# Optimization experiments

Hardware: AMD Instinct MI355X
Metric: run time of the kernel (lower is better)

Reference implementation:

```python
import jax, jax.numpy as jnp
import numpy as np
import math

B, S, D, H, L, F = 32, 512, 512, 8, 4, 1024
TD = 4 * D  # time embedding dim
DH = D // H
SCALE = 1.0 / math.sqrt(DH)


def _ln(x, g, b):
    m = jnp.mean(x, -1, keepdims=True)
    v = jnp.var(x, -1, keepdims=True)
    return (x - m) * jax.lax.rsqrt(v + 1e-5) * g + b


def setup_inputs() -> dict:
    key = jax.random.key(0)
    ks = jax.random.split(key, 12)
    w = lambda k, shp: jax.random.normal(k, shp, dtype=jnp.float32) * 0.02
    return {
        "x": jax.random.normal(ks[0], (B, S, D), dtype=jnp.float32),
        "time": jax.random.uniform(ks[1], (B,), dtype=jnp.float32) * 1000.0,
        "time_w1": w(ks[2], (TD, D)), "time_b1": jnp.zeros((TD,), jnp.float32),
        "time_w2": w(ks[3], (TD, TD)), "time_b2": jnp.zeros((TD,), jnp.float32),
        "Wq": w(ks[4], (L, D, D)), "bq": jnp.zeros((L, D), jnp.float32),
        "Wk": w(ks[5], (L, D, D)), "bk": jnp.zeros((L, D), jnp.float32),
        "Wv": w(ks[6], (L, D, D)), "bv": jnp.zeros((L, D), jnp.float32),
        "Wo": w(ks[7], (L, D, D)), "bo": jnp.zeros((L, D), jnp.float32),
        "attn_g": jnp.ones((L, D), jnp.float32), "attn_b": jnp.zeros((L, D), jnp.float32),
        "ffn_g": jnp.ones((L, D), jnp.float32), "ffn_b": jnp.zeros((L, D), jnp.float32),
        "W1": w(ks[8], (L, 2 * F, D)), "b1": jnp.zeros((L, 2 * F), jnp.float32),
        "W2": w(ks[9], (L, D, F)), "b2": jnp.zeros((L, D), jnp.float32),
        "Wt": w(ks[10], (L, 4 * F, TD)), "bt": jnp.zeros((L, 4 * F), jnp.float32),
        "head_g": jnp.ones((D,), jnp.float32), "head_b": jnp.zeros((D,), jnp.float32),
        "Wh": w(ks[11], (D, D)), "bh": jnp.zeros((D,), jnp.float32),
    }


def _forward(x, time, time_w1, time_b1, time_w2, time_b2,
             Wq, bq, Wk, bk, Wv, bv, Wo, bo,
             attn_g, attn_b, ffn_g, ffn_b,
             W1, b1, W2, b2, Wt, bt,
             head_g, head_b, Wh, bh):
    Bsz = x.shape[0]
    # --- sinusoidal time embedding + time MLP ---
    half = D // 2
    freqs = jnp.exp(jnp.arange(half, dtype=jnp.float32) * (-math.log(10000.0) / (half - 1)))
    e = time[:, None] * freqs[None, :]
    temb = jnp.concatenate([jnp.sin(e), jnp.cos(e)], axis=-1)  # [B, D]
    temb = jax.nn.gelu(temb @ time_w1.T + time_b1, approximate=False) @ time_w2.T + time_b2  # [B, 4D]
    for i in range(L):
        # attention (prenorm; block 0 skips the norm since first_prenormalization=False)
        h = x if i == 0 else _ln(x, attn_g[i], attn_b[i])
        q = (h @ Wq[i].T + bq[i]).reshape(Bsz, S, H, DH)
        k = (h @ Wk[i].T + bk[i]).reshape(Bsz, S, H, DH)
        v = (h @ Wv[i].T + bv[i]).reshape(Bsz, S, H, DH)
        logits = jnp.einsum('bqhd,bkhd->bhqk', q, k) * SCALE
        probs = jax.nn.softmax(logits, axis=-1)
        o = jnp.einsum('bhqk,bkhd->bqhd', probs, v).reshape(Bsz, S, D)
        x = x + (o @ Wo[i].T + bo[i])
        # FFN with FiLM time conditioning and ReGLU activation
        h = _ln(x, ffn_g[i], ffn_b[i])
        h1 = h @ W1[i].T + b1[i]  # [B, S, 2F]
        tm = jax.nn.silu(temb) @ Wt[i].T + bt[i]  # [B, 4F]
        scale, shift = jnp.split(tm[:, None, :], 2, axis=-1)  # each [B, 1, 2F]
        h1 = h1 * (scale + 1.0) + shift
        a, g = jnp.split(h1, 2, axis=-1)  # ReGLU: a * relu(g)
        x = x + ((a * jax.nn.relu(g)) @ W2[i].T + b2[i])
    # head: last token -> LayerNorm -> ReLU -> Linear
    z = _ln(x[:, -1], head_g, head_b)
    return jax.nn.relu(z) @ Wh.T + bh


def reference(x, time, time_w1, time_b1, time_w2, time_b2,
              Wq, bq, Wk, bk, Wv, bv, Wo, bo,
              attn_g, attn_b, ffn_g, ffn_b,
              W1, b1, W2, b2, Wt, bt,
              head_g, head_b, Wh, bh):
    return _forward(x, time, time_w1, time_b1, time_w2, time_b2,
                    Wq, bq, Wk, bk, Wv, bv, Wo, bo,
                    attn_g, attn_b, ffn_g, ffn_b,
                    W1, b1, W2, b2, Wt, bt,
                    head_g, head_b, Wh, bh)
```

## Files before the change

### kernel.cpp

```cpp
#include <hip/hip_runtime.h>
#include <math.h>

typedef __bf16 bf16_t;
typedef __bf16 bf16x8 __attribute__((ext_vector_type(8)));
typedef float f32x4 __attribute__((ext_vector_type(4)));

__device__ __forceinline__ void gload_lds16(const void* g, void* l) {
    __builtin_amdgcn_global_load_lds(
        (const __attribute__((address_space(1))) void*)g,
        (__attribute__((address_space(3))) void*)l, 16, 0, 0);
}

__global__ void k_f2b(const float* __restrict__ in, bf16_t* __restrict__ out, int n8) {
    int idx = blockIdx.x * 256 + threadIdx.x;
    if (idx >= n8) return;
    const float* p = in + (size_t)idx * 8;
    bf16x8 r;
#pragma unroll
    for (int j = 0; j < 8; j++) r[j] = (bf16_t)p[j];
    *(bf16x8*)(out + (size_t)idx * 8) = r;
}

__global__ void k_f2b_s(const float* __restrict__ in, bf16_t* __restrict__ out,
                        int seg8, int dstride8) {
    int idx = blockIdx.x * 256 + threadIdx.x;
    int seg = idx / seg8, rem = idx - seg * seg8;
    const float* p = in + (size_t)idx * 8;
    bf16x8 r;
#pragma unroll
    for (int j = 0; j < 8; j++) r[j] = (bf16_t)p[j];
    *(bf16x8*)(out + ((size_t)seg * dstride8 + rem) * 8) = r;
}

__global__ void k_time_embed(const float* __restrict__ time, float* __restrict__ temb0) {
    int b = blockIdx.x;
    int j = threadIdx.x;
    float f = __expf((float)j * -0.036118981458730134f);
    float e = time[b] * f;
    temb0[(size_t)b * 512 + j] = sinf(e);
    temb0[(size_t)b * 512 + 256 + j] = cosf(e);
}

template<bool DO_NORM, bool IN32>
__global__ void k_ln(const void* __restrict__ xp, const float* __restrict__ g,
                     const float* __restrict__ b, bf16_t* __restrict__ out) {
    int row = blockIdx.x * 4 + (threadIdx.x >> 6);
    int lane = threadIdx.x & 63;
    float vals[8];
    if (IN32) {
        const float* xr = (const float*)xp + (size_t)row * 512 + lane * 8;
        float4 v0 = *(const float4*)xr;
        float4 v1 = *(const float4*)(xr + 4);
        vals[0] = v0.x; vals[1] = v0.y; vals[2] = v0.z; vals[3] = v0.w;
        vals[4] = v1.x; vals[5] = v1.y; vals[6] = v1.z; vals[7] = v1.w;
    } else {
        bf16x8 xv = *(const bf16x8*)((const bf16_t*)xp + (size_t)row * 512 + lane * 8);
#pragma unroll
        for (int j = 0; j < 8; j++) vals[j] = (float)xv[j];
    }
    bf16x8 r;
    if (DO_NORM) {
        float s = 0.f, sq = 0.f;
#pragma unroll
        for (int j = 0; j < 8; j++) { s += vals[j]; sq += vals[j] * vals[j]; }
#pragma unroll
        for (int m = 1; m < 64; m <<= 1) { s += __shfl_xor(s, m, 64); sq += __shfl_xor(sq, m, 64); }
        float mean = s * (1.0f / 512.0f);
        float var = sq * (1.0f / 512.0f) - mean * mean;
        float rstd = rsqrtf(var + 1e-5f);
        float4 g0 = *(const float4*)(g + lane * 8);
        float4 g1 = *(const float4*)(g + lane * 8 + 4);
        float4 b0 = *(const float4*)(b + lane * 8);
        float4 b1 = *(const float4*)(b + lane * 8 + 4);
        float gs[8] = {g0.x, g0.y, g0.z, g0.w, g1.x, g1.y, g1.z, g1.w};
        float bs[8] = {b0.x, b0.y, b0.z, b0.w, b1.x, b1.y, b1.z, b1.w};
#pragma unroll
        for (int j = 0; j < 8; j++) r[j] = (bf16_t)((vals[j] - mean) * rstd * gs[j] + bs[j]);
    } else {
#pragma unroll
        for (int j = 0; j < 8; j++) r[j] = (bf16_t)vals[j];
    }
    *(bf16x8*)(out + (size_t)row * 512 + lane * 8) = r;
}

__global__ void k_head_prep(const bf16_t* __restrict__ x, const float* __restrict__ g,
                            const float* __restrict__ b, float* __restrict__ z) {
    int row = blockIdx.x * 4 + (threadIdx.x >> 6);
    int lane = threadIdx.x & 63;
    bf16x8 xv = *(const bf16x8*)(x + ((size_t)row * 512 + 511) * 512 + lane * 8);
    float vals[8];
#pragma unroll
    for (int j = 0; j < 8; j++) vals[j] = (float)xv[j];
    float s = 0.f, sq = 0.f;
#pragma unroll
    for (int j = 0; j < 8; j++) { s += vals[j]; sq += vals[j] * vals[j]; }
#pragma unroll
    for (int m = 1; m < 64; m <<= 1) { s += __shfl_xor(s, m, 64); sq += __shfl_xor(sq, m, 64); }
    float mean = s * (1.0f / 512.0f);
    float var = sq * (1.0f / 512.0f) - mean * mean;
    float rstd = rsqrtf(var + 1e-5f);
    float o[8];
#pragma unroll
    for (int j = 0; j < 8; j++) {
        float gv = g[lane * 8 + j], bv = b[lane * 8 + j];
        o[j] = fmaxf((vals[j] - mean) * rstd * gv + bv, 0.0f);
    }
    float* zr = z + (size_t)row * 512 + lane * 8;
    *(float4*)zr = make_float4(o[0], o[1], o[2], o[3]);
    *(float4*)(zr + 4) = make_float4(o[4], o[5], o[6], o[7]);
}

template<int ACT, int K, bool OUTB>
__global__ __launch_bounds__(256, 2)
void k_gemm_tm(const float* __restrict__ A, const float* __restrict__ W,
               const float* __restrict__ bias, void* __restrict__ outp, int N) {
    __shared__ float Asm[32][516];
    const int t = threadIdx.x;
    const int kq = t & 7, rw = (t >> 3) & 7, bh = t >> 6;
    const int n0 = blockIdx.x * 32;
    float acc[4][8] = {};
    for (int k0 = 0; k0 < K; k0 += 512) {
        __syncthreads();
#pragma unroll
        for (int i = 0; i < 16; i++) {
            int fid = t + i * 256;
            int row = fid >> 7, cc = (fid & 127) << 2;
            *(float4*)&Asm[row][cc] = *(const float4*)&A[(size_t)row * K + k0 + cc];
        }
        __syncthreads();
#pragma unroll 4
        for (int j = 0; j < 16; j++) {
            int kk = kq * 4 + j * 32;
            float4 w4[4];
#pragma unroll
            for (int r = 0; r < 4; r++)
                w4[r] = *(const float4*)&W[(size_t)(n0 + rw + r * 8) * K + k0 + kk];
#pragma unroll
            for (int b = 0; b < 8; b++) {
                float4 a4 = *(const float4*)&Asm[bh * 8 + b][kk];
#pragma unroll
                for (int r = 0; r < 4; r++)
                    acc[r][b] += a4.x * w4[r].x + a4.y * w4[r].y + a4.z * w4[r].z + a4.w * w4[r].w;
            }
        }
    }
#pragma unroll
    for (int m = 1; m < 8; m <<= 1)
#pragma unroll
        for (int r = 0; r < 4; r++)
#pragma unroll
            for (int b = 0; b < 8; b++)
                acc[r][b] += __shfl_xor(acc[r][b], m, 64);
    if (kq == 0) {
#pragma unroll
        for (int r = 0; r < 4; r++) {
            int n = n0 + rw + r * 8;
            float bv = bias[n];
#pragma unroll
            for (int b = 0; b < 8; b++) {
                float v = acc[r][b] + bv;
                if (ACT == 1) v = 0.5f * v * (1.0f + erff(v * 0.70710678118654752f));
                if (ACT == 2) v = v / (1.0f + __expf(-v));
                if (OUTB) ((bf16_t*)outp)[(size_t)(bh * 8 + b) * N + n] = (bf16_t)v;
                else      ((float*)outp)[(size_t)(bh * 8 + b) * N + n] = v;
            }
        }
    }
}

__global__ void k_fill_tmt(const float* __restrict__ bt, float* __restrict__ tm_t) {
    int i = blockIdx.x * 256 + threadIdx.x;
    tm_t[i] = bt[i >> 5];
}

__global__ __launch_bounds__(256, 4)
void k_gemm_wt(const float* __restrict__ Wt, const bf16_t* __restrict__ t2s_b,
               float* __restrict__ tm_t) {
    __shared__ __align__(16) bf16_t Abuf[64 * 64];
    __shared__ __align__(16) bf16_t Bbuf[32 * 64];
    const int tid = threadIdx.x;
    const int m0 = blockIdx.x * 64;
    const int k0 = blockIdx.y * 512;
    const int lane = tid & 63, wave = tid >> 6;
    const int arow = tid >> 2, aseg = tid & 3;
    const int brow = tid >> 3, bseg = tid & 7;
    const int aswz = (arow & 7) << 4;
    const char* Bg = (const char*)t2s_b + (size_t)brow * 4096 + ((bseg * 16) ^ ((brow & 7) << 4));
    char* BbL = (char*)Bbuf + tid * 16;
    const float* Ar0 = Wt + (size_t)(m0 + arow) * 2048 + k0 + aseg * 16;
    f32x4 acc[2] = {};
    for (int kk0 = 0; kk0 < 512; kk0 += 64) {
        float4 a4[4];
#pragma unroll
        for (int i = 0; i < 4; i++) a4[i] = *(const float4*)(Ar0 + kk0 + i * 4);
        __syncthreads();
        gload_lds16(Bg + (size_t)(k0 + kk0) * 2, BbL);
        bf16x8 c0, c1;
#pragma unroll
        for (int i = 0; i < 4; i++) {
            const float* af = (const float*)&a4[i];
#pragma unroll
            for (int j = 0; j < 4; j++) {
                if (i < 2) c0[i * 4 + j] = (bf16_t)af[j];
                else       c1[(i - 2) * 4 + j] = (bf16_t)af[j];
            }
        }
        int base = arow * 128 + aseg * 32;
        *(bf16x8*)((char*)Abuf + (base ^ aswz)) = c0;
        *(bf16x8*)((char*)Abuf + ((base + 16) ^ aswz)) = c1;
        __syncthreads();
#pragma unroll
        for (int kk = 0; kk < 2; kk++) {
            int ar = wave * 16 + (lane & 15);
            bf16x8 af = *(const bf16x8*)((const char*)Abuf + ar * 128 +
                        ((kk * 64 + (lane >> 4) * 16) ^ ((ar & 7) << 4)));
#pragma unroll
            for (int j = 0; j < 2; j++) {
                int br = j * 16 + (lane & 15);
                bf16x8 bfr = *(const bf16x8*)((const char*)Bbuf + br * 128 +
                             ((kk * 64 + (lane >> 4) * 16) ^ ((br & 7) << 4)));
                acc[j] = __builtin_amdgcn_mfma_f32_16x16x32_bf16(af, bfr, acc[j], 0, 0, 0);
            }
        }
    }
#pragma unroll
    for (int j = 0; j < 2; j++)
#pragma unroll
        for (int r = 0; r < 4; r++) {
            int mrow = m0 + wave * 16 + (lane >> 4) * 4 + r;
            atomicAdd(&tm_t[(size_t)mrow * 32 + j * 16 + (lane & 15)], acc[j][r]);
        }
}

enum { EPI_QKV = 0, EPI_RESID = 1, EPI_FILMGLU = 2 };

template<int EPI, int K, int NBY, int BM, bool RS32>
__global__ __launch_bounds__(BM * 2, 4)
void k_gemm_bt(const bf16_t* __restrict__ A, const bf16_t* __restrict__ W,
               const float* __restrict__ bias, const float* __restrict__ bias2,
               const float* __restrict__ bias3,
               void* __restrict__ out0, const void* __restrict__ rsp, void* __restrict__ out2,
               const float* __restrict__ tm) {
    constexpr int T   = BM * 2;
    constexpr int RPR = BM / 4;
    constexpr int BR  = 512 / BM;
    __shared__ __align__(16) bf16_t Abuf[BM * 64];
    __shared__ __align__(16) bf16_t Bbuf[128 * 64];
    const int tid = threadIdx.x;
    const int cpx = gridDim.x >> 3;
    const int wg = (blockIdx.x & 7) * cpx + (blockIdx.x >> 3);
    const int bx = wg / NBY;
    const int by = wg - bx * NBY;
    const int m0 = bx * BM;
    const int lane = tid & 63;
    const int wid = tid >> 6;
    const int wrM = (wid >> 1) * 64;
    const int wN  = wid & 1;
    const int wc  = wN * 64;

    const int srow = tid >> 3;
    const int goff = ((tid & 7) * 16) ^ ((srow & 7) << 4);
    const char* Ag = (const char*)A;
    const char* Wg = (const char*)W;
    char* AbL = (char*)Abuf + tid * 16;
    char* BbL = (char*)Bbuf + tid * 16;
    int growB[BR];
#pragma unroll
    for (int i = 0; i < BR; i++) {
        int r = srow + i * RPR;
        if (EPI == EPI_FILMGLU) {
            int half = (r >> 5) & 1;
            int base = by * 64 + (r >> 6) * 32 + (r & 31);
            growB[i] = half * 1024 + base;
        } else {
            growB[i] = by * 128 + r;
        }
    }

    f32x4 acc[4][4] = {};
    for (int k0 = 0; k0 < K * 2; k0 += 128) {
        __syncthreads();
#pragma unroll
        for (int i = 0; i < 4; i++)
            gload_lds16(Ag + (size_t)(m0 + srow + i * RPR) * (K * 2) + k0 + goff, AbL + i * (T * 16));
#pragma unroll
        for (int i = 0; i < BR; i++)
            gload_lds16(Wg + (size_t)growB[i] * (K * 2) + k0 + goff, BbL + i * (T * 16));
        __syncthreads();
#pragma unroll
        for (int kk = 0; kk < 2; kk++) {
            bf16x8 af[4], bfr[4];
#pragma unroll
            for (int i = 0; i < 4; i++) {
                int ar = wrM + i * 16 + (lane & 15);
                af[i] = *(const bf16x8*)((const char*)Abuf + ar * 128 +
                         ((kk * 64 + (lane >> 4) * 16) ^ ((ar & 7) << 4)));
                int br = wc + i * 16 + (lane & 15);
                bfr[i] = *(const bf16x8*)((const char*)Bbuf + br * 128 +
                         ((kk * 64 + (lane >> 4) * 16) ^ ((br & 7) << 4)));
            }
#pragma unroll
            for (int i = 0; i < 4; i++)
#pragma unroll
                for (int j = 0; j < 4; j++)
                    acc[i][j] = __builtin_amdgcn_mfma_f32_16x16x32_bf16(af[i], bfr[j], acc[i][j], 0, 0, 0);
        }
    }

    const int b = m0 >> 9;
    if (EPI == EPI_QKV) {
        const int which = by >> 2;
        bf16_t* op = (bf16_t*)(which == 0 ? out0 : which == 1 ? (void*)rsp : out2);
        const float* bp = which == 0 ? bias : which == 1 ? bias2 : bias3;
#pragma unroll
        for (int i = 0; i < 4; i++) {
#pragma unroll
            for (int r = 0; r < 4; r++) {
                int s = (m0 + wrM + i * 16 + (lane >> 4) * 4 + r) & 511;
#pragma unroll
                for (int j = 0; j < 4; j++) {
                    int c = (by & 3) * 128 + wc + j * 16 + (lane & 15);
                    float v = acc[i][j][r] + bp[c];
                    int h = c >> 6, dh = c & 63;
                    op[(((size_t)b * 8 + h) * 512 + s) * 64 + dh] = (bf16_t)v;
                }
            }
        }
    } else if (EPI == EPI_RESID) {
        bf16_t* op = (bf16_t*)out0;
#pragma unroll
        for (int i = 0; i < 4; i++) {
#pragma unroll
            for (int r = 0; r < 4; r++) {
                int row = m0 + wrM + i * 16 + (lane >> 4) * 4 + r;
#pragma unroll
                for (int j = 0; j < 4; j++) {
                    int col = by * 128 + wc + j * 16 + (lane & 15);
                    size_t idx = (size_t)row * 512 + col;
                    float rsv = RS32 ? ((const float*)rsp)[idx] : (float)((const bf16_t*)rsp)[idx];
                    op[idx] = (bf16_t)(rsv + acc[i][j][r] + bias[col]);
                }
            }
        }
    } else {
        bf16_t* op = (bf16_t*)out0;
#pragma unroll
        for (int i = 0; i < 4; i++) {
#pragma unroll
            for (int r = 0; r < 4; r++) {
                int row = m0 + wrM + i * 16 + (lane >> 4) * 4 + r;
#pragma unroll
                for (int jj = 0; jj < 2; jj++) {
                    int colA = by * 64 + wN * 32 + jj * 16 + (lane & 15);
                    float av = acc[i][jj][r] + bias[colA];
                    float gv = acc[i][jj + 2][r] + bias[1024 + colA];
                    float sa = tm[(size_t)colA * 32 + b];
                    float ha = tm[(size_t)(2048 + colA) * 32 + b];
                    float sg = tm[(size_t)(1024 + colA) * 32 + b];
                    float hg = tm[(size_t)(3072 + colA) * 32 + b];
                    av = av * (1.0f + sa) + ha;
                    gv = gv * (1.0f + sg) + hg;
                    op[(size_t)row * 1024 + colA] = (bf16_t)(av * fmaxf(gv, 0.0f));
                }
            }
        }
    }
}

__global__ __launch_bounds__(256, 2)
void k_attn(const bf16_t* __restrict__ q, const bf16_t* __restrict__ k,
            const bf16_t* __restrict__ v, bf16_t* __restrict__ o) {
    __shared__ bf16_t q_lds[64][72];
    __shared__ bf16_t k_lds[64][72];
    __shared__ bf16_t vt_lds[64 * 72];
    __shared__ bf16_t p_lds[64][72];
    const int tid = threadIdx.x;
    const int lane = tid & 63;
    const int wave = tid >> 6;
    const int cpx = gridDim.x >> 3;
    const int wg = ((int)blockIdx.x & 7) * cpx + ((int)blockIdx.x >> 3);
    const int bh = wg >> 3;
    const int qt = wg & 7;
    const bf16_t* qb = q + ((size_t)bh * 512 + qt * 64) * 64;
    const bf16_t* kb = k + (size_t)bh * 512 * 64;
    const bf16_t* vb = v + (size_t)bh * 512 * 64;
    const int sr = tid >> 2;
    const int sc = (tid & 3) * 16;
    {
        bf16x8 a0 = *(const bf16x8*)(qb + sr * 64 + sc);
        bf16x8 a1 = *(const bf16x8*)(qb + sr * 64 + sc + 8);
        bf16x8 ra, rb;
#pragma unroll
        for (int j = 0; j < 8; j++) {
            ra[j] = (bf16_t)((float)a0[j] * 0.125f);
            rb[j] = (bf16_t)((float)a1[j] * 0.125f);
        }
        *(bf16x8*)&q_lds[sr][sc] = ra;
        *(bf16x8*)&q_lds[sr][sc + 8] = rb;
    }
    bf16x8 kr0, kr1, vr0, vr1;
    {
        const bf16_t* ks = kb + (size_t)sr * 64 + sc;
        const bf16_t* vs = vb + (size_t)sr * 64 + sc;
        kr0 = *(const bf16x8*)ks; kr1 = *(const bf16x8*)(ks + 8);
        vr0 = *(const bf16x8*)vs; vr1 = *(const bf16x8*)(vs + 8);
    }
    float mrow[4], lrow[4];
    f32x4 oacc[4] = {};
#pragma unroll
    for (int r = 0; r < 4; r++) { mrow[r] = -1e30f; lrow[r] = 0.f; }
    const int swz0 = ((sc >> 3) & 7) << 4;
    const int swz1 = (((sc + 8) >> 3) & 7) << 4;
    for (int kt = 0; kt < 8; kt++) {
        __syncthreads();
        {
            *(bf16x8*)&k_lds[sr][sc] = kr0;
            *(bf16x8*)&k_lds[sr][sc + 8] = kr1;
            char* vbase = (char*)vt_lds;
            int so0 = (sr * 2) ^ swz0;
            int so1 = (sr * 2) ^ swz1;
#pragma unroll
            for (int j = 0; j < 8; j++) {
                *(bf16_t*)(vbase + (sc + j) * 144 + so0) = vr0[j];
                *(bf16_t*)(vbase + (sc + 8 + j) * 144 + so1) = vr1[j];
            }
        }
        __syncthreads();
        if (kt < 7) {
            const bf16_t* ks = kb + ((size_t)(kt + 1) * 64 + sr) * 64 + sc;
            const bf16_t* vs = vb + ((size_t)(kt + 1) * 64 + sr) * 64 + sc;
            kr0 = *(const bf16x8*)ks; kr1 = *(const bf16x8*)(ks + 8);
            vr0 = *(const bf16x8*)vs; vr1 = *(const bf16x8*)(vs + 8);
        }
        f32x4 sacc[4] = {};
#pragma unroll
        for (int kk = 0; kk < 2; kk++) {
            bf16x8 aq = *(const bf16x8*)&q_lds[wave * 16 + (lane & 15)][kk * 32 + (lane >> 4) * 8];
#pragma unroll
            for (int c = 0; c < 4; c++) {
                bf16x8 bk8 = *(const bf16x8*)&k_lds[c * 16 + (lane & 15)][kk * 32 + (lane >> 4) * 8];
                sacc[c] = __builtin_amdgcn_mfma_f32_16x16x32_bf16(aq, bk8, sacc[c], 0, 0, 0);
            }
        }
#pragma unroll
        for (int r = 0; r < 4; r++) {
            float mx = fmaxf(fmaxf(sacc[0][r], sacc[1][r]), fmaxf(sacc[2][r], sacc[3][r]));
#pragma unroll
            for (int m = 1; m < 16; m <<= 1) mx = fmaxf(mx, __shfl_xor(mx, m, 64));
            float newm = fmaxf(mrow[r], mx);
            float fsc = __expf(mrow[r] - newm);
            mrow[r] = newm;
            float p0 = __expf(sacc[0][r] - newm);
            float p1 = __expf(sacc[1][r] - newm);
            float p2 = __expf(sacc[2][r] - newm);
            float p3 = __expf(sacc[3][r] - newm);
            float ps = p0 + p1 + p2 + p3;
#pragma unroll
            for (int m = 1; m < 16; m <<= 1) ps += __shfl_xor(ps, m, 64);
            lrow[r] = lrow[r] * fsc + ps;
#pragma unroll
            for (int c = 0; c < 4; c++) oacc[c][r] *= fsc;
            int qrow = wave * 16 + (lane >> 4) * 4 + r;
            p_lds[qrow][(lane & 15)] = (bf16_t)p0;
            p_lds[qrow][16 + (lane & 15)] = (bf16_t)p1;
            p_lds[qrow][32 + (lane & 15)] = (bf16_t)p2;
            p_lds[qrow][48 + (lane & 15)] = (bf16_t)p3;
        }
#pragma unroll
        for (int kk = 0; kk < 2; kk++) {
            bf16x8 ap = *(const bf16x8*)&p_lds[wave * 16 + (lane & 15)][kk * 32 + (lane >> 4) * 8];
#pragma unroll
            for (int c = 0; c < 4; c++) {
                int d0 = c * 16 + (lane & 15);
                int xo = ((d0 >> 3) & 7) << 4;
                bf16x8 bv8 = *(const bf16x8*)((const char*)vt_lds + d0 * 144 +
                              ((kk * 64 + (lane >> 4) * 16) ^ xo));
                oacc[c] = __builtin_amdgcn_mfma_f32_16x16x32_bf16(ap, bv8, oacc[c], 0, 0, 0);
            }
        }
    }
    const int b = bh >> 3, h = bh & 7;
#pragma unroll
    for (int r = 0; r < 4; r++) {
        int s = qt * 64 + wave * 16 + (lane >> 4) * 4 + r;
        float inv = 1.0f / lrow[r];
#pragma unroll
        for (int c = 0; c < 4; c++) {
            o[((size_t)b * 512 + s) * 512 + h * 64 + c * 16 + (lane & 15)] = (bf16_t)(oacc[c][r] * inv);
        }
    }
}

extern "C" void kernel_launch(void* const* d_in, const int* in_sizes, int n_in,
                              void* d_out, int out_size, void* d_ws, size_t ws_size,
                              hipStream_t stream) {
    const float* x_in   = (const float*)d_in[0];
    const float* time_in= (const float*)d_in[1];
    const float* tw1    = (const float*)d_in[2];
    const float* tb1    = (const float*)d_in[3];
    const float* tw2    = (const float*)d_in[4];
    const float* tb2    = (const float*)d_in[5];
    const float* Wq     = (const float*)d_in[6];
    const float* bq     = (const float*)d_in[7];
    const float* Wk     = (const float*)d_in[8];
    const float* bk     = (const float*)d_in[9];
    const float* Wv     = (const float*)d_in[10];
    const float* bv     = (const float*)d_in[11];
    const float* Wo     = (const float*)d_in[12];
    const float* bo     = (const float*)d_in[13];
    const float* attn_g = (const float*)d_in[14];
    const float* attn_b = (const float*)d_in[15];
    const float* ffn_g  = (const float*)d_in[16];
    const float* ffn_b  = (const float*)d_in[17];
    const float* W1     = (const float*)d_in[18];
    const float* b1     = (const float*)d_in[19];
    const float* W2     = (const float*)d_in[20];
    const float* b2     = (const float*)d_in[21];
    const float* Wt     = (const float*)d_in[22];
    const float* bt     = (const float*)d_in[23];
    const float* head_g = (const float*)d_in[24];
    const float* head_b = (const float*)d_in[25];
    const float* Wh     = (const float*)d_in[26];
    const float* bh     = (const float*)d_in[27];

    size_t off = 0;
    auto alloc = [&](size_t bytes) {
        void* r = (char*)d_ws + off;
        off += (bytes + 255) & ~(size_t)255;
        return r;
    };
    bf16_t* wqkv_b = (bf16_t*)alloc((size_t)4 * 3 * 512 * 512 * 2);
    bf16_t* wo_b   = (bf16_t*)alloc((size_t)4 * 512 * 512 * 2);
    bf16_t* w1_b   = (bf16_t*)alloc((size_t)4 * 2048 * 512 * 2);
    bf16_t* w2_b   = (bf16_t*)alloc((size_t)4 * 512 * 1024 * 2);
    bf16_t* x_ws   = (bf16_t*)alloc((size_t)16384 * 512 * 2);
    bf16_t* h_b    = (bf16_t*)alloc((size_t)16384 * 512 * 2);
    bf16_t* q_b    = (bf16_t*)alloc((size_t)16384 * 512 * 2);
    bf16_t* k_b    = (bf16_t*)alloc((size_t)16384 * 512 * 2);
    bf16_t* v_b    = (bf16_t*)alloc((size_t)16384 * 512 * 2);
    bf16_t* o_b    = (bf16_t*)alloc((size_t)16384 * 512 * 2);
    bf16_t* act_b  = (bf16_t*)alloc((size_t)16384 * 1024 * 2);
    float*  temb0  = (float*)alloc((size_t)32 * 512 * 4);
    float*  t1     = (float*)alloc((size_t)32 * 2048 * 4);
    bf16_t* t2s_b  = (bf16_t*)alloc((size_t)32 * 2048 * 2);
    float*  tm_t   = (float*)alloc((size_t)16384 * 32 * 4);
    float*  z      = (float*)alloc((size_t)32 * 512 * 4);

    k_f2b_s<<<512, 256, 0, stream>>>(Wq, wqkv_b,          32768, 98304);
    k_f2b_s<<<512, 256, 0, stream>>>(Wk, wqkv_b + 262144, 32768, 98304);
    k_f2b_s<<<512, 256, 0, stream>>>(Wv, wqkv_b + 524288, 32768, 98304);
    k_f2b<<<512, 256, 0, stream>>>(Wo, wo_b, 131072);
    k_f2b<<<2048, 256, 0, stream>>>(W1, w1_b, 524288);
    k_f2b<<<1024, 256, 0, stream>>>(W2, w2_b, 262144);

    k_time_embed<<<32, 256, 0, stream>>>(time_in, temb0);
    k_gemm_tm<1, 512, false><<<64, 256, 0, stream>>>(temb0, tw1, tb1, t1, 2048);
    k_gemm_tm<2, 2048, true><<<64, 256, 0, stream>>>(t1, tw2, tb2, t2s_b, 2048);
    k_fill_tmt<<<2048, 256, 0, stream>>>(bt, tm_t);
    k_gemm_wt<<<dim3(256, 4), 256, 0, stream>>>(Wt, t2s_b, tm_t);

    for (int l = 0; l < 4; l++) {
        if (l == 0)
            k_ln<false, true><<<4096, 256, 0, stream>>>(x_in, nullptr, nullptr, h_b);
        else
            k_ln<true, false><<<4096, 256, 0, stream>>>(x_ws, attn_g + l * 512, attn_b + l * 512, h_b);

        k_gemm_bt<EPI_QKV, 512, 12, 256, false><<<768, 512, 0, stream>>>(
            h_b, wqkv_b + (size_t)l * 786432,
            bq + l * 512, bk + l * 512, bv + l * 512,
            q_b, k_b, v_b, nullptr);

        k_attn<<<2048, 256, 0, stream>>>(q_b, k_b, v_b, o_b);

        if (l == 0)
            k_gemm_bt<EPI_RESID, 512, 4, 128, true><<<512, 256, 0, stream>>>(
                o_b, wo_b + (size_t)l * 262144,
                bo + l * 512, nullptr, nullptr,
                x_ws, x_in, nullptr, nullptr);
        else
            k_gemm_bt<EPI_RESID, 512, 4, 128, false><<<512, 256, 0, stream>>>(
                o_b, wo_b + (size_t)l * 262144,
                bo + l * 512, nullptr, nullptr,
                x_ws, x_ws, nullptr, nullptr);

        k_ln<true, false><<<4096, 256, 0, stream>>>(x_ws, ffn_g + l * 512, ffn_b + l * 512, h_b);

        k_gemm_bt<EPI_FILMGLU, 512, 16, 256, false><<<1024, 512, 0, stream>>>(
            h_b, w1_b + (size_t)l * 1048576,
            b1 + l * 2048, nullptr, nullptr,
            act_b, nullptr, nullptr, tm_t + (size_t)l * 4096 * 32);

        k_gemm_bt<EPI_RESID, 1024, 4, 128, false><<<512, 256, 0, stream>>>(
            act_b, w2_b + (size_t)l * 524288,
            b2 + l * 512, nullptr, nullptr,
            x_ws, x_ws, nullptr, nullptr);
    }

    k_head_prep<<<8, 256, 0, stream>>>(x_ws, head_g, head_b, z);
    k_gemm_tm<0, 512, false><<<16, 256, 0, stream>>>(z, Wh, bh, (float*)d_out, 512);
}
```

Baseline: 1.092 ms.

## Replace block-shared GEMM tiles with per-wave double-buffered LDS pipeline

```diff
diff --git a/kernel.cpp b/kernel.cpp
--- a/kernel.cpp
+++ b/kernel.cpp
@@ -234,78 +234,84 @@
 
 enum { EPI_QKV = 0, EPI_RESID = 1, EPI_FILMGLU = 2 };
 
-template<int EPI, int K, int NBY, int BM, bool RS32>
-__global__ __launch_bounds__(BM * 2, 4)
-void k_gemm_bt(const bf16_t* __restrict__ A, const bf16_t* __restrict__ W,
+template<int EPI, int K, int NBY, bool RS32>
+__global__ __launch_bounds__(256, 2)
+void k_gemm_wp(const bf16_t* __restrict__ A, const bf16_t* __restrict__ W,
                const float* __restrict__ bias, const float* __restrict__ bias2,
                const float* __restrict__ bias3,
                void* __restrict__ out0, const void* __restrict__ rsp, void* __restrict__ out2,
                const float* __restrict__ tm) {
-    constexpr int T   = BM * 2;
-    constexpr int RPR = BM / 4;
-    constexpr int BR  = 512 / BM;
-    __shared__ __align__(16) bf16_t Abuf[BM * 64];
-    __shared__ __align__(16) bf16_t Bbuf[128 * 64];
+    __shared__ __align__(16) char lds_raw[4][2][8192];
     const int tid = threadIdx.x;
     const int cpx = gridDim.x >> 3;
     const int wg = (blockIdx.x & 7) * cpx + (blockIdx.x >> 3);
     const int bx = wg / NBY;
     const int by = wg - bx * NBY;
-    const int m0 = bx * BM;
+    const int m0 = bx * 128;
     const int lane = tid & 63;
     const int wid = tid >> 6;
     const int wrM = (wid >> 1) * 64;
     const int wN  = wid & 1;
     const int wc  = wN * 64;
 
-    const int srow = tid >> 3;
-    const int goff = ((tid & 7) * 16) ^ ((srow & 7) << 4);
+    const int srw  = lane >> 2;
+    const int cswz = (((lane & 3) ^ (srw & 3)) << 4);
     const char* Ag = (const char*)A;
     const char* Wg = (const char*)W;
-    char* AbL = (char*)Abuf + tid * 16;
-    char* BbL = (char*)Bbuf + tid * 16;
-    int growB[BR];
-#pragma unroll
-    for (int i = 0; i < BR; i++) {
-        int r = srow + i * RPR;
+    size_t arowoff[4], browoff[4];
+#pragma unroll
+    for (int i = 0; i < 4; i++) {
+        arowoff[i] = (size_t)(m0 + wrM + i * 16 + srw) * (K * 2);
+        int rb = wc + i * 16 + srw;
+        int grow;
         if (EPI == EPI_FILMGLU) {
-            int half = (r >> 5) & 1;
-            int base = by * 64 + (r >> 6) * 32 + (r & 31);
-            growB[i] = half * 1024 + base;
+            int half = (rb >> 5) & 1;
+            grow = half * 1024 + by * 64 + (rb >> 6) * 32 + (rb & 31);
         } else {
-            growB[i] = by * 128 + r;
-        }
-    }
+            grow = by * 128 + rb;
+        }
+        browoff[i] = (size_t)grow * (K * 2);
+    }
+
+    auto stage = [&](int buf, int t) {
+        const int k0 = t * 64;
+        char* dst = lds_raw[wid][buf] + lane * 16;
+#pragma unroll
+        for (int i = 0; i < 4; i++)
+            gload_lds16(Ag + arowoff[i] + k0 + cswz, dst + i * 1024);
+#pragma unroll
+        for (int i = 0; i < 4; i++)
+            gload_lds16(Wg + browoff[i] + k0 + cswz, dst + 4096 + i * 1024);
+    };
 
     f32x4 acc[4][4] = {};
-    for (int k0 = 0; k0 < K * 2; k0 += 128) {
-        __syncthreads();
+    const int rdswz = (((lane >> 4) ^ (lane & 3)) << 4);
+    auto compute = [&](int buf) {
+        const char* ra = lds_raw[wid][buf];
+        const char* rb = ra + 4096;
+        bf16x8 af[4], bf[4];
+#pragma unroll
+        for (int i = 0; i < 4; i++) {
+            af[i] = *(const bf16x8*)(ra + (i * 16 + (lane & 15)) * 64 + rdswz);
+            bf[i] = *(const bf16x8*)(rb + (i * 16 + (lane & 15)) * 64 + rdswz);
+        }
 #pragma unroll
         for (int i = 0; i < 4; i++)
-            gload_lds16(Ag + (size_t)(m0 + srow + i * RPR) * (K * 2) + k0 + goff, AbL + i * (T * 16));
-#pragma unroll
-        for (int i = 0; i < BR; i++)
-            gload_lds16(Wg + (size_t)growB[i] * (K * 2) + k0 + goff, BbL + i * (T * 16));
-        __syncthreads();
-#pragma unroll
-        for (int kk = 0; kk < 2; kk++) {
-            bf16x8 af[4], bfr[4];
-#pragma unroll
-            for (int i = 0; i < 4; i++) {
-                int ar = wrM + i * 16 + (lane & 15);
-                af[i] = *(const bf16x8*)((const char*)Abuf + ar * 128 +
-                         ((kk * 64 + (lane >> 4) * 16) ^ ((ar & 7) << 4)));
-                int br = wc + i * 16 + (lane & 15);
-                bfr[i] = *(const bf16x8*)((const char*)Bbuf + br * 128 +
-                         ((kk * 64 + (lane >> 4) * 16) ^ ((br & 7) << 4)));
-            }
-#pragma unroll
-            for (int i = 0; i < 4; i++)
-#pragma unroll
-                for (int j = 0; j < 4; j++)
-                    acc[i][j] = __builtin_amdgcn_mfma_f32_16x16x32_bf16(af[i], bfr[j], acc[i][j], 0, 0, 0);
-        }
-    }
+#pragma unroll
+            for (int j = 0; j < 4; j++)
+                acc[i][j] = __builtin_amdgcn_mfma_f32_16x16x32_bf16(af[i], bf[j], acc[i][j], 0, 0, 0);
+        asm volatile("s_waitcnt lgkmcnt(0)" ::: "memory");
+    };
+
+    const int NT = K / 32;
+    stage(0, 0);
+    for (int t = 0; t < NT - 1; ++t) {
+        stage((t + 1) & 1, t + 1);
+        asm volatile("s_waitcnt vmcnt(8)" ::: "memory");
+        compute(t & 1);
+    }
+    asm volatile("s_waitcnt vmcnt(0)" ::: "memory");
+    compute((NT - 1) & 1);
 
     const int b = m0 >> 9;
     if (EPI == EPI_QKV) {
@@ -565,7 +571,7 @@
         else
             k_ln<true, false><<<4096, 256, 0, stream>>>(x_ws, attn_g + l * 512, attn_b + l * 512, h_b);
 
-        k_gemm_bt<EPI_QKV, 512, 12, 256, false><<<768, 512, 0, stream>>>(
+        k_gemm_wp<EPI_QKV, 512, 12, false><<<1536, 256, 0, stream>>>(
             h_b, wqkv_b + (size_t)l * 786432,
             bq + l * 512, bk + l * 512, bv + l * 512,
             q_b, k_b, v_b, nullptr);
@@ -573,24 +579,24 @@
         k_attn<<<2048, 256, 0, stream>>>(q_b, k_b, v_b, o_b);
 
         if (l == 0)
-            k_gemm_bt<EPI_RESID, 512, 4, 128, true><<<512, 256, 0, stream>>>(
+            k_gemm_wp<EPI_RESID, 512, 4, true><<<512, 256, 0, stream>>>(
                 o_b, wo_b + (size_t)l * 262144,
                 bo + l * 512, nullptr, nullptr,
                 x_ws, x_in, nullptr, nullptr);
         else
-            k_gemm_bt<EPI_RESID, 512, 4, 128, false><<<512, 256, 0, stream>>>(
+            k_gemm_wp<EPI_RESID, 512, 4, false><<<512, 256, 0, stream>>>(
                 o_b, wo_b + (size_t)l * 262144,
                 bo + l * 512, nullptr, nullptr,
                 x_ws, x_ws, nullptr, nullptr);
 
         k_ln<true, false><<<4096, 256, 0, stream>>>(x_ws, ffn_g + l * 512, ffn_b + l * 512, h_b);
 
-        k_gemm_bt<EPI_FILMGLU, 512, 16, 256, false><<<1024, 512, 0, stream>>>(
+        k_gemm_wp<EPI_FILMGLU, 512, 16, false><<<2048, 256, 0, stream>>>(
             h_b, w1_b + (size_t)l * 1048576,
             b1 + l * 2048, nullptr, nullptr,
             act_b, nullptr, nullptr, tm_t + (size_t)l * 4096 * 32);
 
-        k_gemm_bt<EPI_RESID, 1024, 4, 128, false><<<512, 256, 0, stream>>>(
+        k_gemm_wp<EPI_RESID, 1024, 4, false><<<512, 256, 0, stream>>>(
             act_b, w2_b + (size_t)l * 524288,
             b2 + l * 512, nullptr, nullptr,
             x_ws, x_ws, nullptr, nullptr);
```

Result: slower. 1.230 ms (+12.6%).
